# Kernel tuning notes

Hardware: AMD Instinct MI355X
Metric: run time of the kernel (lower is better)

Reference implementation:

```python
import jax, jax.numpy as jnp
import numpy as np

D_MODEL = 1024
NUM_HEADS = 16
D_HEAD = D_MODEL // NUM_HEADS
B, T = 2, 2048


def setup_inputs() -> dict:
    key = jax.random.key(0)
    kx, kq, kk, kv, ko = jax.random.split(key, 5)
    # xavier_uniform bound for square (D,D) linear weights
    bound = float(np.sqrt(6.0 / (D_MODEL + D_MODEL)))
    uni = lambda k: jax.random.uniform(k, (D_MODEL, D_MODEL), jnp.float32, -bound, bound)
    return {
        "x": jax.random.normal(kx, (B, T, D_MODEL), jnp.float32),
        "Wq": uni(kq),
        "Wk": uni(kk),
        "Wv": uni(kv),
        "Wo": uni(ko),
    }


def _split_heads(x):
    # (B, T, D) -> (B, H, T, d_head)
    b, t, _ = x.shape
    return x.reshape(b, t, NUM_HEADS, D_HEAD).transpose(0, 2, 1, 3)


def _exclusive_output_mod(Y, V):
    dt = V.dtype
    tiny = jnp.asarray(jnp.finfo(dt).tiny, dt)
    eps = jnp.asarray(jnp.finfo(dt).eps, dt)
    v_sq = jnp.sum(V * V, axis=-1, keepdims=True)
    y_dot_v = jnp.sum(Y * V, axis=-1, keepdims=True)
    scale = jnp.where(v_sq > 0, y_dot_v / jnp.maximum(v_sq, tiny), jnp.zeros_like(y_dot_v))
    Z = Y - scale * V
    residual_norm = jnp.linalg.norm(Z, axis=-1, keepdims=True)
    reference_norm = jnp.maximum(
        jnp.linalg.norm(Y, axis=-1, keepdims=True),
        jnp.linalg.norm(V, axis=-1, keepdims=True),
    )
    cleanup_tol = eps * Z.shape[-1] * reference_norm
    return jnp.where((v_sq > 0) & (residual_norm <= cleanup_tol), jnp.zeros_like(Z), Z)


def reference(x, Wq, Wk, Wv, Wo):
    Q = _split_heads(x @ Wq.T)  # (B,H,T,dh)
    K = _split_heads(x @ Wk.T)
    V = _split_heads(x @ Wv.T)
    sm_scale = 1.0 / np.sqrt(D_HEAD)
    scores = jnp.einsum("bhqd,bhkd->bhqk", Q, K) * sm_scale
    P = jax.nn.softmax(scores, axis=-1)
    Y = jnp.einsum("bhqk,bhkd->bhqd", P, V)
    Z = _exclusive_output_mod(Y, V)
    # merge heads: (B,H,T,dh) -> (B,T,D)
    Zm = Z.transpose(0, 2, 1, 3).reshape(x.shape[0], x.shape[1], D_MODEL)
    return Zm @ Wo.T
```

## Files before the change

### kernel.cpp

```cpp
#include <hip/hip_runtime.h>
#include <math.h>

#define DM   1024
#define TTOK 2048
#define NTOK 4096

typedef __bf16 bf16x8 __attribute__((ext_vector_type(8)));
typedef __bf16 bf16x4 __attribute__((ext_vector_type(4)));
typedef float  f32x4  __attribute__((ext_vector_type(4)));
typedef float  f32x16 __attribute__((ext_vector_type(16)));

#define QSCALE 0.18033688011112042f

#if defined(__has_builtin)
#if __has_builtin(__builtin_amdgcn_exp2f)
#define EXP2F(x) __builtin_amdgcn_exp2f(x)
#endif
#endif
#ifndef EXP2F
#define EXP2F(x) exp2f(x)
#endif

#define GLDS16(g, l) __builtin_amdgcn_global_load_lds( \
    (__attribute__((address_space(1))) void*)(g),      \
    (__attribute__((address_space(3))) void*)(l), 16, 0, 0)

__global__ __launch_bounds__(256)
void cvt_all(const float* __restrict__ x,  const float* __restrict__ Wq,
             const float* __restrict__ Wk, const float* __restrict__ Wv,
             const float* __restrict__ Wo, __bf16* __restrict__ dst) {
    size_t g = ((size_t)blockIdx.x * 256 + threadIdx.x) * 8;
    const float* s;
    size_t off;
    const size_t NX = (size_t)NTOK * DM;
    if (g < NX) { s = x; off = g; }
    else {
        size_t gg = g - NX;
        int w = (int)(gg >> 20);
        off = gg & ((1u << 20) - 1);
        s = (w == 0) ? Wq : (w == 1) ? Wk : (w == 2) ? Wv : Wo;
    }
    float4 a = *(const float4*)(s + off);
    float4 b = *(const float4*)(s + off + 4);
    bf16x8 v;
    v[0] = (__bf16)a.x; v[1] = (__bf16)a.y; v[2] = (__bf16)a.z; v[3] = (__bf16)a.w;
    v[4] = (__bf16)b.x; v[5] = (__bf16)b.y; v[6] = (__bf16)b.z; v[7] = (__bf16)b.w;
    *(bf16x8*)(dst + g) = v;
}

#define LSTR 136

template<int MODE>
__global__ __launch_bounds__(256)
void gemm_bf16(const __bf16* __restrict__ X,
               const __bf16* __restrict__ W0, const __bf16* __restrict__ W1,
               const __bf16* __restrict__ W2,
               __bf16* __restrict__ Oq, __bf16* __restrict__ Ok,
               __bf16* __restrict__ Ovt, float* __restrict__ Of)
{
    const int z = (MODE == 0) ? blockIdx.z : 3;
    const __bf16 *A, *B;
    int m0, n0;
    if (MODE == 0 && z < 2) {
        A = z ? W1 : W0; B = X;
        m0 = blockIdx.y * 128; n0 = blockIdx.x * 128;
    } else if (MODE == 0) {
        A = X; B = W2;
        m0 = blockIdx.x * 128; n0 = blockIdx.y * 128;
    } else {
        A = X; B = W0;
        m0 = blockIdx.y * 128; n0 = blockIdx.x * 128;
    }

    __shared__ __attribute__((aligned(16))) __bf16 smem[128 * LSTR];
    __bf16* As = smem;
    __bf16* Bs = smem + 128 * 32;

    const int tid  = threadIdx.x;
    const int lane = tid & 63;
    const int wave = tid >> 6;
    const int wm = wave & 1, wn = wave >> 1;
    const int col = lane & 15, quad = lane >> 4;

    const __bf16* Ag = A + (size_t)(m0 + (tid >> 2)) * DM + (tid & 3) * 8;
    const __bf16* Bg = B + (size_t)(n0 + (tid >> 2)) * DM + (tid & 3) * 8;
    __bf16* lA = As + tid * 8;
    __bf16* lB = Bs + tid * 8;

    f32x4 acc[4][4];
#pragma unroll
    for (int i = 0; i < 4; ++i)
#pragma unroll
        for (int j = 0; j < 4; ++j)
#pragma unroll
            for (int r = 0; r < 4; ++r) acc[i][j][r] = 0.0f;

    for (int k0 = 0; k0 < DM; k0 += 32) {
        __syncthreads();
        GLDS16(Ag + k0,                   lA);
        GLDS16(Ag + (size_t)64 * DM + k0, lA + 2048);
        GLDS16(Bg + k0,                   lB);
        GLDS16(Bg + (size_t)64 * DM + k0, lB + 2048);
        __syncthreads();
        bf16x8 af[4], bfr[4];
#pragma unroll
        for (int i = 0; i < 4; ++i)
            af[i] = *(const bf16x8*)&As[(wm * 64 + i * 16 + col) * 32 + quad * 8];
#pragma unroll
        for (int j = 0; j < 4; ++j)
            bfr[j] = *(const bf16x8*)&Bs[(wn * 64 + j * 16 + col) * 32 + quad * 8];
#pragma unroll
        for (int i = 0; i < 4; ++i)
#pragma unroll
            for (int j = 0; j < 4; ++j)
                acc[i][j] = __builtin_amdgcn_mfma_f32_16x16x32_bf16(af[i], bfr[j], acc[i][j], 0, 0, 0);
    }

    if (MODE == 1) {
#pragma unroll
        for (int i = 0; i < 4; ++i)
#pragma unroll
            for (int j = 0; j < 4; ++j) {
                const int mb = m0 + wm * 64 + i * 16 + quad * 4;
                const int n  = n0 + wn * 64 + j * 16 + col;
#pragma unroll
                for (int r = 0; r < 4; ++r)
                    Of[(size_t)(mb + r) * DM + n] = acc[i][j][r];
            }
        return;
    }

    const float sc = (z == 0) ? QSCALE : 1.0f;
    __syncthreads();
#pragma unroll
    for (int i = 0; i < 4; ++i)
#pragma unroll
        for (int j = 0; j < 4; ++j) {
            const int ml = wm * 64 + i * 16 + quad * 4;
            const int nl = wn * 64 + j * 16 + col;
            bf16x4 pk;
#pragma unroll
            for (int r = 0; r < 4; ++r) pk[r] = (__bf16)(acc[i][j][r] * sc);
            *(bf16x4*)&smem[nl * LSTR + ml] = pk;
        }
    __syncthreads();

#pragma unroll
    for (int it = 0; it < 8; ++it) {
        int c   = tid + 256 * it;
        int row = c >> 4;
        int ch  = (c & 15) * 8;
        bf16x8 v = *(const bf16x8*)&smem[row * LSTR + ch];
        if (z < 2) {
            int t  = n0 + row;
            int b  = t >> 11; t &= 2047;
            int hd = m0 + ch;
            int h  = hd >> 6, d = hd & 63;
            *(bf16x8*)&((z ? Ok : Oq)[(((size_t)(b * 16 + h)) * TTOK + t) * 64 + d]) = v;
        } else {
            int hd = n0 + row;
            int h  = hd >> 6, d = hd & 63;
            int t  = m0 + ch;
            int b  = t >> 11; t &= 2047;
            *(bf16x8*)&Ovt[(((size_t)(b * 16 + h)) * 64 + d) * TTOK + t] = v;
        }
    }
}

__global__ __launch_bounds__(256)
void attn_mfma(const __bf16* __restrict__ Qg, const __bf16* __restrict__ Kg,
               const __bf16* __restrict__ Vtg, __bf16* __restrict__ Zm)
{
    const int bh = blockIdx.y;
    const int q0 = blockIdx.x * 128;
    const size_t base = (size_t)bh * TTOK * 64;

    __shared__ __attribute__((aligned(16))) __bf16 Ks[64 * 72];
    __shared__ __attribute__((aligned(16))) __bf16 Vs[64 * 72];
    __shared__ __attribute__((aligned(16))) __bf16 QPs[128 * 72];

    const int tid  = threadIdx.x;
    const int lane = tid & 63, wave = tid >> 6;
    const int c32  = lane & 31, h32 = lane >> 5;

#pragma unroll
    for (int it = 0; it < 2; ++it) {
        int idx = tid + 256 * it;
        int r = idx >> 2, off = (idx & 3) * 16;
        const __bf16* src = Qg + base + (size_t)(q0 + r) * 64 + off;
        *(bf16x8*)&QPs[r * 72 + off]     = *(const bf16x8*)(src);
        *(bf16x8*)&QPs[r * 72 + off + 8] = *(const bf16x8*)(src + 8);
    }
    __syncthreads();
    bf16x8 qf[4];
#pragma unroll
    for (int st = 0; st < 4; ++st)
        qf[st] = *(const bf16x8*)&QPs[(wave * 32 + c32) * 72 + h32 * 8 + st * 16];

    bf16x8 ones;
#pragma unroll
    for (int i = 0; i < 8; ++i) ones[i] = (__bf16)1.0f;

    f32x16 O[2], lacc;
#pragma unroll
    for (int r = 0; r < 16; ++r) { O[0][r] = 0.0f; O[1][r] = 0.0f; lacc[r] = 0.0f; }

    const int rs = tid >> 2, soff = (tid & 3) * 16;

    bf16x8 kr0 = *(const bf16x8*)(Kg  + base + (size_t)rs * 64 + soff);
    bf16x8 kr1 = *(const bf16x8*)(Kg  + base + (size_t)rs * 64 + soff + 8);
    bf16x8 vr0 = *(const bf16x8*)(Vtg + base + (size_t)rs * TTOK + soff);
    bf16x8 vr1 = *(const bf16x8*)(Vtg + base + (size_t)rs * TTOK + soff + 8);

    const int kb_tgt = (q0 >> 6) + (wave >> 1);
    const int qo     = (wave & 1) * 32 + c32;
    float vq[2][16];

    for (int kb = 0; kb < TTOK / 64; ++kb) {
        __syncthreads();
        *(bf16x8*)&Ks[rs * 72 + soff]     = kr0;
        *(bf16x8*)&Ks[rs * 72 + soff + 8] = kr1;
        *(bf16x8*)&Vs[rs * 72 + soff]     = vr0;
        *(bf16x8*)&Vs[rs * 72 + soff + 8] = vr1;
        __syncthreads();

        {
            int kbn = (kb + 1) & (TTOK / 64 - 1);
            const __bf16* kp = Kg  + base + (size_t)(kbn * 64 + rs) * 64 + soff;
            const __bf16* vp = Vtg + base + (size_t)rs * TTOK + kbn * 64 + soff;
            kr0 = *(const bf16x8*)(kp); kr1 = *(const bf16x8*)(kp + 8);
            vr0 = *(const bf16x8*)(vp); vr1 = *(const bf16x8*)(vp + 8);
        }

        f32x16 s0, s1;
#pragma unroll
        for (int r = 0; r < 16; ++r) { s0[r] = 0.0f; s1[r] = 0.0f; }
#pragma unroll
        for (int st = 0; st < 4; ++st) {
            bf16x8 a0 = *(const bf16x8*)&Ks[(c32)      * 72 + h32 * 8 + st * 16];
            bf16x8 a1 = *(const bf16x8*)&Ks[(32 + c32) * 72 + h32 * 8 + st * 16];
            s0 = __builtin_amdgcn_mfma_f32_32x32x16_bf16(a0, qf[st], s0, 0, 0, 0);
            s1 = __builtin_amdgcn_mfma_f32_32x32x16_bf16(a1, qf[st], s1, 0, 0, 0);
        }

#pragma unroll
        for (int kb2 = 0; kb2 < 2; ++kb2) {
#pragma unroll
            for (int g = 0; g < 4; ++g) {
                float p0 = EXP2F(kb2 ? s1[4 * g + 0] : s0[4 * g + 0]);
                float p1 = EXP2F(kb2 ? s1[4 * g + 1] : s0[4 * g + 1]);
                float p2 = EXP2F(kb2 ? s1[4 * g + 2] : s0[4 * g + 2]);
                float p3 = EXP2F(kb2 ? s1[4 * g + 3] : s0[4 * g + 3]);
                bf16x4 pk;
                pk[0] = (__bf16)p0; pk[1] = (__bf16)p1;
                pk[2] = (__bf16)p2; pk[3] = (__bf16)p3;
                *(bf16x4*)&QPs[(wave * 32 + c32) * 72 + kb2 * 32 + g * 8 + h32 * 4] = pk;
            }
        }

#pragma unroll
        for (int ks = 0; ks < 4; ++ks) {
            bf16x8 pf = *(const bf16x8*)&QPs[(wave * 32 + c32) * 72 + h32 * 8 + ks * 16];
            lacc = __builtin_amdgcn_mfma_f32_32x32x16_bf16(ones, pf, lacc, 0, 0, 0);
            bf16x8 v0 = *(const bf16x8*)&Vs[(c32)      * 72 + h32 * 8 + ks * 16];
            bf16x8 v1 = *(const bf16x8*)&Vs[(32 + c32) * 72 + h32 * 8 + ks * 16];
            O[0] = __builtin_amdgcn_mfma_f32_32x32x16_bf16(v0, pf, O[0], 0, 0, 0);
            O[1] = __builtin_amdgcn_mfma_f32_32x32x16_bf16(v1, pf, O[1], 0, 0, 0);
        }

        if (kb == kb_tgt) {
#pragma unroll
            for (int db = 0; db < 2; ++db)
#pragma unroll
                for (int rg = 0; rg < 16; ++rg) {
                    int d = db * 32 + (rg & 3) + 8 * (rg >> 2) + 4 * h32;
                    vq[db][rg] = (float)Vs[d * 72 + qo];
                }
        }
    }

    const float inv = 1.0f / lacc[0];

    const int b = bh >> 4, h = bh & 15;
    const int q = q0 + wave * 32 + c32;
    float y[2][16];
    float yv = 0.f, v2 = 0.f, yy = 0.f;
#pragma unroll
    for (int db = 0; db < 2; ++db)
#pragma unroll
        for (int rg = 0; rg < 16; ++rg) {
            float yval = O[db][rg] * inv;
            float vval = vq[db][rg];
            y[db][rg] = yval;
            yv += yval * vval; v2 += vval * vval; yy += yval * yval;
        }
    yv += __shfl_xor(yv, 32, 64);
    v2 += __shfl_xor(v2, 32, 64);
    yy += __shfl_xor(yy, 32, 64);
    float scl = (v2 > 0.0f) ? yv / fmaxf(v2, 1.1754943508222875e-38f) : 0.0f;
    float zz = 0.f;
    float zvv[2][16];
#pragma unroll
    for (int db = 0; db < 2; ++db)
#pragma unroll
        for (int rg = 0; rg < 16; ++rg) {
            zvv[db][rg] = y[db][rg] - scl * vq[db][rg];
            zz += zvv[db][rg] * zvv[db][rg];
        }
    zz += __shfl_xor(zz, 32, 64);
    float znorm = sqrtf(zz);
    float refn  = fmaxf(sqrtf(yy), sqrtf(v2));
    bool  wipe  = (v2 > 0.0f) && (znorm <= 1.1920928955078125e-07f * 64.0f * refn);
#pragma unroll
    for (int db = 0; db < 2; ++db)
#pragma unroll
        for (int g = 0; g < 4; ++g) {
            bf16x4 pk;
#pragma unroll
            for (int r = 0; r < 4; ++r)
                pk[r] = (__bf16)(wipe ? 0.0f : zvv[db][4 * g + r]);
            int d = db * 32 + 8 * g + 4 * h32;
            *(bf16x4*)&Zm[((size_t)(b * TTOK + q)) * DM + h * 64 + d] = pk;
        }
}

extern "C" void kernel_launch(void* const* d_in, const int* in_sizes, int n_in,
                              void* d_out, int out_size, void* d_ws, size_t ws_size,
                              hipStream_t stream) {
    const float* x  = (const float*)d_in[0];
    const float* Wq = (const float*)d_in[1];
    const float* Wk = (const float*)d_in[2];
    const float* Wv = (const float*)d_in[3];
    const float* Wo = (const float*)d_in[4];

    const size_t NX = (size_t)NTOK * DM;
    const size_t NW = (size_t)DM * DM;
    __bf16* xb  = (__bf16*)d_ws;
    __bf16* wqb = xb  + NX;
    __bf16* wkb = wqb + NW;
    __bf16* wvb = wkb + NW;
    __bf16* wob = wvb + NW;
    __bf16* Qb  = wob + NW;
    __bf16* Kb  = Qb  + NX;
    __bf16* Vtb = Kb  + NX;
    __bf16* Zmb = Vtb + NX;

    cvt_all<<<(NX + 4 * NW) / 2048, 256, 0, stream>>>(x, Wq, Wk, Wv, Wo, xb);

    gemm_bf16<0><<<dim3(32, 8, 3), 256, 0, stream>>>(
        xb, wqb, wkb, wvb, Qb, Kb, Vtb, nullptr);

    attn_mfma<<<dim3(TTOK / 128, 32), 256, 0, stream>>>(Qb, Kb, Vtb, Zmb);

    gemm_bf16<1><<<dim3(8, 32), 256, 0, stream>>>(
        Zmb, wob, nullptr, nullptr, nullptr, nullptr, nullptr, (float*)d_out);
}
```

Measured before the change: 192.6 us.

## Double-buffer GEMM LDS tiles and raise wave priority around attention MFMAs

The GEMM main loop now uses two LDS buffers: it issues global-to-LDS loads for the next K tile before computing on the current one, and needs one barrier per iteration instead of two. This hides global load latency behind MFMA work. Separately, the attention kernel wraps its QK and PV MFMA blocks in s_setprio(1)/s_setprio(0) so the scheduler favours waves issuing matrix ops. A risk is correctness: the async LDS loads into the next buffer may not have completed when the trailing __syncthreads runs, since there is no explicit vmcnt wait.

```diff
diff --git a/kernel.cpp b/kernel.cpp
--- a/kernel.cpp
+++ b/kernel.cpp
@@ -49,6 +49,7 @@
 }
 
 #define LSTR 136
+#define DBUF 8192
 
 template<int MODE>
 __global__ __launch_bounds__(256)
@@ -73,8 +74,6 @@
     }
 
     __shared__ __attribute__((aligned(16))) __bf16 smem[128 * LSTR];
-    __bf16* As = smem;
-    __bf16* Bs = smem + 128 * 32;
 
     const int tid  = threadIdx.x;
     const int lane = tid & 63;
@@ -84,8 +83,8 @@
 
     const __bf16* Ag = A + (size_t)(m0 + (tid >> 2)) * DM + (tid & 3) * 8;
     const __bf16* Bg = B + (size_t)(n0 + (tid >> 2)) * DM + (tid & 3) * 8;
-    __bf16* lA = As + tid * 8;
-    __bf16* lB = Bs + tid * 8;
+    __bf16* lA = smem + tid * 8;
+    __bf16* lB = smem + 4096 + tid * 8;
 
     f32x4 acc[4][4];
 #pragma unroll
@@ -95,25 +94,41 @@
 #pragma unroll
             for (int r = 0; r < 4; ++r) acc[i][j][r] = 0.0f;
 
-    for (int k0 = 0; k0 < DM; k0 += 32) {
-        __syncthreads();
-        GLDS16(Ag + k0,                   lA);
-        GLDS16(Ag + (size_t)64 * DM + k0, lA + 2048);
-        GLDS16(Bg + k0,                   lB);
-        GLDS16(Bg + (size_t)64 * DM + k0, lB + 2048);
-        __syncthreads();
+    GLDS16(Ag,                   lA);
+    GLDS16(Ag + (size_t)64 * DM, lA + 2048);
+    GLDS16(Bg,                   lB);
+    GLDS16(Bg + (size_t)64 * DM, lB + 2048);
+    __syncthreads();
+
+    const int nk = DM / 32;
+    for (int t = 0; t < nk; ++t) {
+        const int cur = (t & 1) * DBUF;
+        const int nxt = DBUF - cur;
+
+        if (t + 1 < nk) {
+            const int k1 = (t + 1) * 32;
+            GLDS16(Ag + k1,                   lA + nxt);
+            GLDS16(Ag + (size_t)64 * DM + k1, lA + nxt + 2048);
+            GLDS16(Bg + k1,                   lB + nxt);
+            GLDS16(Bg + (size_t)64 * DM + k1, lB + nxt + 2048);
+        }
+
+        const __bf16* Asr = smem + cur;
+        const __bf16* Bsr = smem + cur + 4096;
         bf16x8 af[4], bfr[4];
 #pragma unroll
         for (int i = 0; i < 4; ++i)
-            af[i] = *(const bf16x8*)&As[(wm * 64 + i * 16 + col) * 32 + quad * 8];
+            af[i] = *(const bf16x8*)&Asr[(wm * 64 + i * 16 + col) * 32 + quad * 8];
 #pragma unroll
         for (int j = 0; j < 4; ++j)
-            bfr[j] = *(const bf16x8*)&Bs[(wn * 64 + j * 16 + col) * 32 + quad * 8];
+            bfr[j] = *(const bf16x8*)&Bsr[(wn * 64 + j * 16 + col) * 32 + quad * 8];
 #pragma unroll
         for (int i = 0; i < 4; ++i)
 #pragma unroll
             for (int j = 0; j < 4; ++j)
                 acc[i][j] = __builtin_amdgcn_mfma_f32_16x16x32_bf16(af[i], bfr[j], acc[i][j], 0, 0, 0);
+
+        __syncthreads();
     }
 
     if (MODE == 1) {
@@ -131,7 +146,6 @@
     }
 
     const float sc = (z == 0) ? QSCALE : 1.0f;
-    __syncthreads();
 #pragma unroll
     for (int i = 0; i < 4; ++i)
 #pragma unroll
@@ -235,6 +249,7 @@
         f32x16 s0, s1;
 #pragma unroll
         for (int r = 0; r < 16; ++r) { s0[r] = 0.0f; s1[r] = 0.0f; }
+        __builtin_amdgcn_s_setprio(1);
 #pragma unroll
         for (int st = 0; st < 4; ++st) {
             bf16x8 a0 = *(const bf16x8*)&Ks[(c32)      * 72 + h32 * 8 + st * 16];
@@ -242,6 +257,7 @@
             s0 = __builtin_amdgcn_mfma_f32_32x32x16_bf16(a0, qf[st], s0, 0, 0, 0);
             s1 = __builtin_amdgcn_mfma_f32_32x32x16_bf16(a1, qf[st], s1, 0, 0, 0);
         }
+        __builtin_amdgcn_s_setprio(0);
 
 #pragma unroll
         for (int kb2 = 0; kb2 < 2; ++kb2) {
@@ -258,6 +274,7 @@
             }
         }
 
+        __builtin_amdgcn_s_setprio(1);
 #pragma unroll
         for (int ks = 0; ks < 4; ++ks) {
             bf16x8 pf = *(const bf16x8*)&QPs[(wave * 32 + c32) * 72 + h32 * 8 + ks * 16];
@@ -267,6 +284,7 @@
             O[0] = __builtin_amdgcn_mfma_f32_32x32x16_bf16(v0, pf, O[0], 0, 0, 0);
             O[1] = __builtin_amdgcn_mfma_f32_32x32x16_bf16(v1, pf, O[1], 0, 0, 0);
         }
+        __builtin_amdgcn_s_setprio(0);
 
         if (kb == kb_tgt) {
 #pragma unroll
```

Measured after the change: 195.6 us. Within noise of the previous version (+1.5%).
